# Kernel tuning notes

Measured on AMD Instinct MI355X. Metric: run time of the kernel, lower is better.

Reference implementation:

```python
import jax, jax.numpy as jnp
import numpy as np

DIM = 512
N_HEAD = 4
WIN = (5, 9)

def setup_inputs() -> dict:
    key = jax.random.key(0)
    ks = jax.random.split(key, 9)
    s = DIM ** -0.5
    x = jax.random.normal(ks[0], (1, 8, 60, 108, DIM), jnp.float32)
    Wq = jax.random.normal(ks[1], (DIM, DIM), jnp.float32) * s
    bq = jax.random.normal(ks[2], (DIM,), jnp.float32) * 0.02
    Wk = jax.random.normal(ks[3], (DIM, DIM), jnp.float32) * s
    bk = jax.random.normal(ks[4], (DIM,), jnp.float32) * 0.02
    Wv = jax.random.normal(ks[5], (DIM, DIM), jnp.float32) * s
    bv = jax.random.normal(ks[6], (DIM,), jnp.float32) * 0.02
    Wp = jax.random.normal(ks[7], (DIM, DIM), jnp.float32) * s
    bp = jax.random.normal(ks[8], (DIM,), jnp.float32) * 0.02
    return {"x": x, "Wq": Wq, "bq": bq, "Wk": Wk, "bk": bk,
            "Wv": Wv, "bv": bv, "Wp": Wp, "bp": bp}

def reference(x, Wq, bq, Wk, bk, Wv, bv, Wp, bp):
    b, t, h, w, c = x.shape
    w_h, w_w = WIN
    n_head = N_HEAD
    c_head = c // n_head
    n_wh = -(-h // w_h)
    n_ww = -(-w // w_w)
    new_h, new_w = n_wh * w_h, n_ww * w_w
    pad_b, pad_r = new_h - h, new_w - w
    if pad_b > 0 or pad_r > 0:
        x = jnp.pad(x, ((0, 0), (0, 0), (0, pad_b), (0, pad_r), (0, 0)))
    # torch nn.Linear: y = x @ W.T + b, weight shape (out, in)
    q = jnp.einsum('bthwc,dc->bthwd', x, Wq) + bq
    k = jnp.einsum('bthwc,dc->bthwd', x, Wk) + bk
    v = jnp.einsum('bthwc,dc->bthwd', x, Wv) + bv

    def part(z):
        # (b,t,H,W,c) -> (b, n_windows, n_head, t*w_h*w_w, c_head)
        z = z.reshape(b, t, n_wh, w_h, n_ww, w_w, n_head, c_head)
        z = z.transpose(0, 2, 4, 6, 1, 3, 5, 7)
        return z.reshape(b, n_wh * n_ww, n_head, t * w_h * w_w, c_head)

    qw, kw, vw = part(q), part(k), part(v)
    scale = c_head ** -0.5
    # all (batch, window) attentions batched into one einsum (fused form of the torch double loop)
    scores = jnp.einsum('bwnsc,bwnkc->bwnsk', qw, kw) * scale
    attn = jax.nn.softmax(scores, axis=-1)
    out = jnp.einsum('bwnsk,bwnkc->bwnsc', attn, vw)
    # merge windows back: (b,t,new_h,new_w,c)
    out = out.reshape(b, n_wh, n_ww, n_head, t, w_h, w_w, c_head)
    out = out.transpose(0, 4, 1, 5, 2, 6, 3, 7).reshape(b, t, new_h, new_w, c)
    out = out[:, :, :h, :w, :]
    out = jnp.einsum('bthwc,dc->bthwd', out, Wp) + bp
    return out
```

## Files before the change

### kernel.cpp

```cpp
#include <hip/hip_runtime.h>

typedef _Float16 f16;
typedef _Float16 f16x8 __attribute__((ext_vector_type(8)));
typedef _Float16 f16x4 __attribute__((ext_vector_type(4)));
typedef float f32x4 __attribute__((ext_vector_type(4)));
typedef unsigned int u32;
typedef unsigned int u32x4 __attribute__((ext_vector_type(4)));

#define MFMA16(a, b, c) __builtin_amdgcn_mfma_f32_16x16x32_f16(a, b, c, 0, 0, 0)

__device__ __forceinline__ void async_copy16(f16* lds, const f16* g) {
    __builtin_amdgcn_global_load_lds(
        (const __attribute__((address_space(1))) unsigned int*)g,
        (__attribute__((address_space(3))) unsigned int*)lds,
        16, 0, 0);
}

__global__ __launch_bounds__(256) void prep_convert(
    const float* __restrict__ x, f16* __restrict__ xh,
    const float* __restrict__ Wq, const float* __restrict__ Wk,
    const float* __restrict__ Wv, const float* __restrict__ Wp,
    const float* __restrict__ bq, const float* __restrict__ bk,
    const float* __restrict__ bv,
    f16* __restrict__ Wqkv, f16* __restrict__ Wph, float* __restrict__ bqkv,
    int* __restrict__ tokmap)
{
    if (blockIdx.x < 12960) {
        int i = blockIdx.x * 256 + threadIdx.x;
        f32x4 a = *(const f32x4*)(x + (size_t)i * 8);
        f32x4 b = *(const f32x4*)(x + (size_t)i * 8 + 4);
        f16x8 h = { (f16)a[0], (f16)a[1], (f16)a[2], (f16)a[3],
                    (f16)b[0], (f16)b[1], (f16)b[2], (f16)b[3] };
        *(f16x8*)(xh + (size_t)i * 8) = h;
        return;
    }
    int i = (blockIdx.x - 12960) * 256 + threadIdx.x;
    if (i < 786432) {
        int r = i >> 9, c = i & 511;
        const float* src = (r < 512) ? Wq : (r < 1024) ? Wk : Wv;
        Wqkv[i] = (f16)src[(r & 511) * 512 + c];
    } else if (i < 786432 + 262144) {
        int j = i - 786432;
        Wph[j] = (f16)Wp[j];
    } else if (i < 786432 + 262144 + 1536) {
        int j = i - (786432 + 262144);
        bqkv[j] = (j < 512) ? bq[j] : (j < 1024) ? bk[j - 512] : bv[j - 1024];
    } else if (i < 786432 + 262144 + 1536 + 51840) {
        int j = i - (786432 + 262144 + 1536);
        int t_ = j / 6480, rem = j % 6480;
        int hh = rem / 108, ww = rem % 108;
        int win = (hh / 5) * 12 + (ww / 9);
        int s = t_ * 45 + (hh % 5) * 9 + (ww % 9);
        tokmap[j] = win * 1440 + s;
    }
}

__global__ __launch_bounds__(256, 3) void qkv_gemm(
    const f16* __restrict__ Xh, const f16* __restrict__ W,
    const float* __restrict__ bias, const int* __restrict__ tokmap,
    f16* __restrict__ Qp, f16* __restrict__ Kp, f16* __restrict__ Vp)
{
    __shared__ __align__(16) f16 As[3][128 * 32];
    __shared__ __align__(16) f16 Bs[3][128 * 32];
    const int tid = threadIdx.x;
    const int lane = tid & 63, wid = tid >> 6;
    const int g = lane >> 4, l15 = lane & 15;
    const int wr = wid >> 1, wc = wid & 1;

    const int orig = blockIdx.x;
    const int xcd = orig & 7;
    const int wg = (xcd < 4 ? xcd * 608 : 2432 + (xcd - 4) * 607) + (orig >> 3);
    const int bn = wg % 12;
    const int brow = (wg / 12) * 128;

    const f16* Abase = Xh + (size_t)brow * 512;
    const f16* Bbase = W + (size_t)bn * 128 * 512;

    f32x4 acc[4][4] = {};

    #define QKV_STAGE(buf, step)                                              \
        {                                                                     \
            const int k0_ = (step) * 32;                                      \
            _Pragma("unroll")                                                 \
            for (int rr = 0; rr < 2; ++rr) {                                  \
                int idx = rr * 256 + tid;                                     \
                int row = idx >> 2, ch = idx & 3;                             \
                int sch = ch ^ ((row >> 1) & 3);                              \
                async_copy16(&As[buf][idx * 8],                               \
                             Abase + (size_t)row * 512 + k0_ + sch * 8);      \
                async_copy16(&Bs[buf][idx * 8],                               \
                             Bbase + (size_t)row * 512 + k0_ + sch * 8);      \
            }                                                                 \
        }

    QKV_STAGE(0, 0);
    QKV_STAGE(1, 1);

    int cur = 0;
    for (int t = 0; t < 16; ++t) {
        if (t < 15) asm volatile("s_waitcnt vmcnt(4)" ::: "memory");
        else        asm volatile("s_waitcnt vmcnt(0)" ::: "memory");
        __builtin_amdgcn_s_barrier();
        __builtin_amdgcn_sched_barrier(0);
        if (t + 2 < 16) {
            int stg = cur + 2; if (stg >= 3) stg -= 3;
            QKV_STAGE(stg, t + 2);
        }
        f16x8 a[4], b[4];
        #pragma unroll
        for (int m = 0; m < 4; ++m) {
            int arow = wr * 64 + m * 16 + l15;
            int sl = g ^ ((arow >> 1) & 3);
            a[m] = *(const f16x8*)&As[cur][arow * 32 + sl * 8];
        }
        #pragma unroll
        for (int n = 0; n < 4; ++n) {
            int brw = wc * 64 + n * 16 + l15;
            int sl = g ^ ((brw >> 1) & 3);
            b[n] = *(const f16x8*)&Bs[cur][brw * 32 + sl * 8];
        }
        __builtin_amdgcn_s_setprio(1);
        #pragma unroll
        for (int m = 0; m < 4; ++m)
            #pragma unroll
            for (int n = 0; n < 4; ++n)
                acc[m][n] = MFMA16(a[m], b[n], acc[m][n]);
        __builtin_amdgcn_s_setprio(0);
        __builtin_amdgcn_s_barrier();
        cur = (cur == 2) ? 0 : cur + 1;
    }
    #undef QKV_STAGE

    const int which = bn >> 2, head = bn & 3;
    f16* dst = (which == 0) ? Qp : (which == 1) ? Kp : Vp;
    #pragma unroll
    for (int m = 0; m < 4; ++m) {
        #pragma unroll
        for (int j = 0; j < 4; ++j) {
            int gm = brow + wr * 64 + m * 16 + g * 4 + j;
            size_t obase = ((size_t)(tokmap[gm] + head * 360)) * 128;
            #pragma unroll
            for (int n = 0; n < 4; ++n) {
                int cidx = wc * 64 + n * 16 + l15;
                float v = acc[m][n][j] + bias[bn * 128 + cidx];
                dst[obase + cidx] = (f16)v;
            }
        }
    }
}

__global__ __launch_bounds__(256, 2) void attn_kernel(
    const f16* __restrict__ Qp, const f16* __restrict__ Kp,
    const f16* __restrict__ Vp, f16* __restrict__ AO)
{
    __shared__ __align__(16) f16 Kl[64 * 140];
    __shared__ __align__(16) f16 Vt[128 * 76];
    __shared__ __align__(16) f16 Pl[192 * 76];

    const int tid = threadIdx.x;
    const int lane = tid & 63, wid = tid >> 6;
    const int g = lane >> 4, l15 = lane & 15;
    const int wh = blockIdx.x >> 1;
    const int half = blockIdx.x & 1;
    const int win = wh >> 2, head = wh & 3;
    const int base = wh * 46080;
    const int qbase = half * 192 + wid * 48;

    const float SC2 = 0.08838834764831845f * 1.4426950408889634f;

    f16x8 qf[3][4];
    #pragma unroll
    for (int qi = 0; qi < 3; ++qi)
        #pragma unroll
        for (int c4 = 0; c4 < 4; ++c4)
            qf[qi][c4] = *(const f16x8*)(Qp + base + (qbase + qi * 16 + l15) * 128 + c4 * 32 + g * 8);

    f32x4 o[3][8] = {};
    float l_r[3] = { 0.f, 0.f, 0.f };

    for (int kt = 0; kt < 6; ++kt) {
        #pragma unroll
        for (int it = 0; it < 4; ++it) {
            int idx = it * 256 + tid;
            int krow = idx >> 4, seg = idx & 15;
            f16x8 kv = *(const f16x8*)(Kp + base + (kt * 64 + krow) * 128 + seg * 8);
            *(f16x8*)&Kl[krow * 140 + seg * 8] = kv;
        }
        #pragma unroll
        for (int it = 0; it < 2; ++it) {
            int i2 = it * 256 + tid;
            int kb = i2 >> 6;
            int chp = (i2 & 63) * 2;
            const u32* Vb = (const u32*)(Vp + base);
            u32 d[8];
            #pragma unroll
            for (int i = 0; i < 8; ++i) {
                int kg = kt * 64 + kb * 8 + i;
                d[i] = (kg < 360) ? Vb[kg * 64 + (chp >> 1)] : 0u;
            }
            u32x4 lo, hi;
            #pragma unroll
            for (int jj = 0; jj < 4; ++jj) {
                lo[jj] = (d[2 * jj] & 0xffffu) | (d[2 * jj + 1] << 16);
                hi[jj] = (d[2 * jj] >> 16) | (d[2 * jj + 1] & 0xffff0000u);
            }
            *(u32x4*)&Vt[chp * 76 + kb * 8] = lo;
            *(u32x4*)&Vt[(chp + 1) * 76 + kb * 8] = hi;
        }
        __syncthreads();

        f32x4 sc[4][3] = {};
        __builtin_amdgcn_s_setprio(1);
        #pragma unroll
        for (int c4 = 0; c4 < 4; ++c4) {
            f16x8 ka[4];
            #pragma unroll
            for (int kf = 0; kf < 4; ++kf)
                ka[kf] = *(const f16x8*)&Kl[(kf * 16 + l15) * 140 + c4 * 32 + g * 8];
            #pragma unroll
            for (int kf = 0; kf < 4; ++kf)
                #pragma unroll
                for (int qi = 0; qi < 3; ++qi)
                    sc[kf][qi] = MFMA16(ka[kf], qf[qi][c4], sc[kf][qi]);
        }
        __builtin_amdgcn_s_setprio(0);
        if (kt == 5) {
            #pragma unroll
            for (int kf = 0; kf < 4; ++kf)
                #pragma unroll
                for (int j = 0; j < 4; ++j)
                    if (320 + kf * 16 + g * 4 + j >= 360) {
                        #pragma unroll
                        for (int qi = 0; qi < 3; ++qi) sc[kf][qi][j] = -1e30f;
                    }
        }

        #pragma unroll
        for (int qi = 0; qi < 3; ++qi) {
            float psum = 0.f;
            #pragma unroll
            for (int kf = 0; kf < 4; ++kf) {
                f16x4 pv;
                #pragma unroll
                for (int j = 0; j < 4; ++j) {
                    float p = exp2f(sc[kf][qi][j] * SC2);
                    psum += p;
                    pv[j] = (f16)p;
                }
                *(f16x4*)&Pl[(wid * 48 + qi * 16 + l15) * 76 + kf * 16 + g * 4] = pv;
            }
            psum += __shfl_xor(psum, 16);
            psum += __shfl_xor(psum, 32);
            l_r[qi] += psum;
        }

        __builtin_amdgcn_s_setprio(1);
        #pragma unroll
        for (int kc = 0; kc < 2; ++kc) {
            f16x8 pa[3], vb[8];
            #pragma unroll
            for (int qi = 0; qi < 3; ++qi)
                pa[qi] = *(const f16x8*)&Pl[(wid * 48 + qi * 16 + l15) * 76 + kc * 32 + g * 8];
            #pragma unroll
            for (int chf = 0; chf < 8; ++chf)
                vb[chf] = *(const f16x8*)&Vt[(chf * 16 + l15) * 76 + kc * 32 + g * 8];
            #pragma unroll
            for (int qi = 0; qi < 3; ++qi)
                #pragma unroll
                for (int chf = 0; chf < 8; ++chf)
                    o[qi][chf] = MFMA16(pa[qi], vb[chf], o[qi][chf]);
        }
        __builtin_amdgcn_s_setprio(0);
        __syncthreads();
    }

    #pragma unroll
    for (int qi = 0; qi < 3; ++qi) {
        #pragma unroll
        for (int j = 0; j < 4; ++j) {
            float lj = __shfl(l_r[qi], g * 4 + j);
            float inv = 1.0f / lj;
            int s = qbase + qi * 16 + g * 4 + j;
            if (s < 360) {
                int t_ = s / 45, s45 = s % 45;
                int hh = (win / 12) * 5 + s45 / 9;
                int ww = (win % 12) * 9 + s45 % 9;
                int mm = t_ * 6480 + hh * 108 + ww;
                #pragma unroll
                for (int chf = 0; chf < 8; ++chf) {
                    int col = head * 128 + chf * 16 + l15;
                    AO[(size_t)mm * 512 + col] = (f16)(o[qi][chf][j] * inv);
                }
            }
        }
    }
}

__global__ __launch_bounds__(256, 3) void proj_gemm(
    const f16* __restrict__ A, const f16* __restrict__ W,
    const float* __restrict__ bias, float* __restrict__ out)
{
    __shared__ __align__(16) f16 As[3][128 * 32];
    __shared__ __align__(16) f16 Bs[3][128 * 32];
    const int tid = threadIdx.x;
    const int lane = tid & 63, wid = tid >> 6;
    const int g = lane >> 4, l15 = lane & 15;
    const int wr = wid >> 1, wc = wid & 1;

    const int orig = blockIdx.x;
    const int xcd = orig & 7;
    const int wg = (xcd < 4 ? xcd * 203 : 812 + (xcd - 4) * 202) + (orig >> 3);
    const int bcol = (wg & 3) * 128;
    const int brow = (wg >> 2) * 128;

    const f16* Abase = A + (size_t)brow * 512;
    const f16* Bbase = W + (size_t)bcol * 512;

    f32x4 acc[4][4] = {};

    #define PROJ_STAGE(buf, step)                                             \
        {                                                                     \
            const int k0_ = (step) * 32;                                      \
            _Pragma("unroll")                                                 \
            for (int rr = 0; rr < 2; ++rr) {                                  \
                int idx = rr * 256 + tid;                                     \
                int row = idx >> 2, ch = idx & 3;                             \
                int sch = ch ^ ((row >> 1) & 3);                              \
                async_copy16(&As[buf][idx * 8],                               \
                             Abase + (size_t)row * 512 + k0_ + sch * 8);      \
                async_copy16(&Bs[buf][idx * 8],                               \
                             Bbase + (size_t)row * 512 + k0_ + sch * 8);      \
            }                                                                 \
        }

    PROJ_STAGE(0, 0);
    PROJ_STAGE(1, 1);

    int cur = 0;
    for (int t = 0; t < 16; ++t) {
        if (t < 15) asm volatile("s_waitcnt vmcnt(4)" ::: "memory");
        else        asm volatile("s_waitcnt vmcnt(0)" ::: "memory");
        __builtin_amdgcn_s_barrier();
        __builtin_amdgcn_sched_barrier(0);
        if (t + 2 < 16) {
            int stg = cur + 2; if (stg >= 3) stg -= 3;
            PROJ_STAGE(stg, t + 2);
        }
        f16x8 a[4], b[4];
        #pragma unroll
        for (int m = 0; m < 4; ++m) {
            int arow = wr * 64 + m * 16 + l15;
            int sl = g ^ ((arow >> 1) & 3);
            a[m] = *(const f16x8*)&As[cur][arow * 32 + sl * 8];
        }
        #pragma unroll
        for (int n = 0; n < 4; ++n) {
            int brw = wc * 64 + n * 16 + l15;
            int sl = g ^ ((brw >> 1) & 3);
            b[n] = *(const f16x8*)&Bs[cur][brw * 32 + sl * 8];
        }
        __builtin_amdgcn_s_setprio(1);
        #pragma unroll
        for (int m = 0; m < 4; ++m)
            #pragma unroll
            for (int n = 0; n < 4; ++n)
                acc[m][n] = MFMA16(a[m], b[n], acc[m][n]);
        __builtin_amdgcn_s_setprio(0);
        __builtin_amdgcn_s_barrier();
        cur = (cur == 2) ? 0 : cur + 1;
    }
    #undef PROJ_STAGE

    #pragma unroll
    for (int m = 0; m < 4; ++m)
        #pragma unroll
        for (int j = 0; j < 4; ++j) {
            int gm = brow + wr * 64 + m * 16 + g * 4 + j;
            #pragma unroll
            for (int n = 0; n < 4; ++n) {
                int gn = bcol + wc * 64 + n * 16 + l15;
                out[(size_t)gm * 512 + gn] = acc[m][n][j] + bias[gn];
            }
        }
}

extern "C" void kernel_launch(void* const* d_in, const int* in_sizes, int n_in,
                              void* d_out, int out_size, void* d_ws, size_t ws_size,
                              hipStream_t stream)
{
    (void)in_sizes; (void)n_in; (void)out_size; (void)ws_size;
    const float* x  = (const float*)d_in[0];
    const float* Wq = (const float*)d_in[1];
    const float* bq = (const float*)d_in[2];
    const float* Wk = (const float*)d_in[3];
    const float* bk = (const float*)d_in[4];
    const float* Wv = (const float*)d_in[5];
    const float* bv = (const float*)d_in[6];
    const float* Wp = (const float*)d_in[7];
    const float* bp = (const float*)d_in[8];

    f16* Qp   = (f16*)d_ws;
    f16* Kp   = Qp + 26542080;
    f16* Vp   = Kp + 26542080;
    f16* AO   = Vp + 26542080;
    f16* xh   = AO;
    f16* Wqkv = AO + 26542080;
    f16* Wph  = Wqkv + 786432;
    float* bqkv = (float*)(Wph + 262144);
    int* tokmap = (int*)(bqkv + 1536);

    prep_convert<<<17265, 256, 0, stream>>>(x, xh, Wq, Wk, Wv, Wp, bq, bk, bv,
                                            Wqkv, Wph, bqkv, tokmap);
    qkv_gemm<<<4860, 256, 0, stream>>>(xh, Wqkv, bqkv, tokmap, Qp, Kp, Vp);
    attn_kernel<<<1152, 256, 0, stream>>>(Qp, Kp, Vp, AO);
    proj_gemm<<<1620, 256, 0, stream>>>(AO, Wph, bp, (float*)d_out);
}
```

Measured before the change: 267.7 us.

## Fuse fp32-to-fp16 input conversion into QKV GEMM tile loads

Removes the separate pass that converted x to fp16 and instead streams fp32 x tiles directly into LDS inside the QKV GEMM, converting to fp16 when building MFMA fragments. This eliminates a full read/write pass over the activation tensor and one kernel's worth of work. In exchange the GEMM reads twice as many bytes for A per tile, uses more LDS with a new swizzle, and its occupancy hint drops from 3 to 2 blocks per CU.

```diff
diff --git a/kernel.cpp b/kernel.cpp
--- a/kernel.cpp
+++ b/kernel.cpp
@@ -9,15 +9,14 @@
 
 #define MFMA16(a, b, c) __builtin_amdgcn_mfma_f32_16x16x32_f16(a, b, c, 0, 0, 0)
 
-__device__ __forceinline__ void async_copy16(f16* lds, const f16* g) {
+__device__ __forceinline__ void async_copy16(const void* g, void* lds) {
     __builtin_amdgcn_global_load_lds(
         (const __attribute__((address_space(1))) unsigned int*)g,
         (__attribute__((address_space(3))) unsigned int*)lds,
         16, 0, 0);
 }
 
-__global__ __launch_bounds__(256) void prep_convert(
-    const float* __restrict__ x, f16* __restrict__ xh,
+__global__ __launch_bounds__(256) void prep_kernel(
     const float* __restrict__ Wq, const float* __restrict__ Wk,
     const float* __restrict__ Wv, const float* __restrict__ Wp,
     const float* __restrict__ bq, const float* __restrict__ bk,
@@ -25,16 +24,7 @@
     f16* __restrict__ Wqkv, f16* __restrict__ Wph, float* __restrict__ bqkv,
     int* __restrict__ tokmap)
 {
-    if (blockIdx.x < 12960) {
-        int i = blockIdx.x * 256 + threadIdx.x;
-        f32x4 a = *(const f32x4*)(x + (size_t)i * 8);
-        f32x4 b = *(const f32x4*)(x + (size_t)i * 8 + 4);
-        f16x8 h = { (f16)a[0], (f16)a[1], (f16)a[2], (f16)a[3],
-                    (f16)b[0], (f16)b[1], (f16)b[2], (f16)b[3] };
-        *(f16x8*)(xh + (size_t)i * 8) = h;
-        return;
-    }
-    int i = (blockIdx.x - 12960) * 256 + threadIdx.x;
+    int i = blockIdx.x * 256 + threadIdx.x;
     if (i < 786432) {
         int r = i >> 9, c = i & 511;
         const float* src = (r < 512) ? Wq : (r < 1024) ? Wk : Wv;
@@ -55,12 +45,12 @@
     }
 }
 
-__global__ __launch_bounds__(256, 3) void qkv_gemm(
-    const f16* __restrict__ Xh, const f16* __restrict__ W,
+__global__ __launch_bounds__(256, 2) void qkv_gemm(
+    const float* __restrict__ X, const f16* __restrict__ W,
     const float* __restrict__ bias, const int* __restrict__ tokmap,
     f16* __restrict__ Qp, f16* __restrict__ Kp, f16* __restrict__ Vp)
 {
-    __shared__ __align__(16) f16 As[3][128 * 32];
+    __shared__ __align__(16) float Af[3][128 * 32];
     __shared__ __align__(16) f16 Bs[3][128 * 32];
     const int tid = threadIdx.x;
     const int lane = tid & 63, wid = tid >> 6;
@@ -73,7 +63,7 @@
     const int bn = wg % 12;
     const int brow = (wg / 12) * 128;
 
-    const f16* Abase = Xh + (size_t)brow * 512;
+    const float* Abase = X + (size_t)brow * 512;
     const f16* Bbase = W + (size_t)bn * 128 * 512;
 
     f32x4 acc[4][4] = {};
@@ -81,15 +71,21 @@
     #define QKV_STAGE(buf, step)                                              \
         {                                                                     \
             const int k0_ = (step) * 32;                                      \
+            _Pragma("unroll")                                                 \
+            for (int rr = 0; rr < 4; ++rr) {                                  \
+                int idx = rr * 256 + tid;                                     \
+                int row = idx >> 3, sl = idx & 7;                             \
+                int ss = sl ^ (row & 7);                                      \
+                async_copy16(Abase + (size_t)row * 512 + k0_ + ss * 4,        \
+                             &Af[buf][idx * 4]);                              \
+            }                                                                 \
             _Pragma("unroll")                                                 \
             for (int rr = 0; rr < 2; ++rr) {                                  \
                 int idx = rr * 256 + tid;                                     \
                 int row = idx >> 2, ch = idx & 3;                             \
                 int sch = ch ^ ((row >> 1) & 3);                              \
-                async_copy16(&As[buf][idx * 8],                               \
-                             Abase + (size_t)row * 512 + k0_ + sch * 8);      \
-                async_copy16(&Bs[buf][idx * 8],                               \
-                             Bbase + (size_t)row * 512 + k0_ + sch * 8);      \
+                async_copy16(Bbase + (size_t)row * 512 + k0_ + sch * 8,       \
+                             &Bs[buf][idx * 8]);                              \
             }                                                                 \
         }
 
@@ -98,7 +94,7 @@
 
     int cur = 0;
     for (int t = 0; t < 16; ++t) {
-        if (t < 15) asm volatile("s_waitcnt vmcnt(4)" ::: "memory");
+        if (t < 15) asm volatile("s_waitcnt vmcnt(6)" ::: "memory");
         else        asm volatile("s_waitcnt vmcnt(0)" ::: "memory");
         __builtin_amdgcn_s_barrier();
         __builtin_amdgcn_sched_barrier(0);
@@ -110,8 +106,12 @@
         #pragma unroll
         for (int m = 0; m < 4; ++m) {
             int arow = wr * 64 + m * 16 + l15;
-            int sl = g ^ ((arow >> 1) & 3);
-            a[m] = *(const f16x8*)&As[cur][arow * 32 + sl * 8];
+            int s0 = (2 * g) ^ (arow & 7);
+            int s1 = (2 * g + 1) ^ (arow & 7);
+            f32x4 lo = *(const f32x4*)&Af[cur][arow * 32 + s0 * 4];
+            f32x4 hi = *(const f32x4*)&Af[cur][arow * 32 + s1 * 4];
+            a[m] = f16x8{ (f16)lo[0], (f16)lo[1], (f16)lo[2], (f16)lo[3],
+                          (f16)hi[0], (f16)hi[1], (f16)hi[2], (f16)hi[3] };
         }
         #pragma unroll
         for (int n = 0; n < 4; ++n) {
@@ -326,10 +326,10 @@
                 int idx = rr * 256 + tid;                                     \
                 int row = idx >> 2, ch = idx & 3;                             \
                 int sch = ch ^ ((row >> 1) & 3);                              \
-                async_copy16(&As[buf][idx * 8],                               \
-                             Abase + (size_t)row * 512 + k0_ + sch * 8);      \
-                async_copy16(&Bs[buf][idx * 8],                               \
-                             Bbase + (size_t)row * 512 + k0_ + sch * 8);      \
+                async_copy16(Abase + (size_t)row * 512 + k0_ + sch * 8,       \
+                             &As[buf][idx * 8]);                              \
+                async_copy16(Bbase + (size_t)row * 512 + k0_ + sch * 8,       \
+                             &Bs[buf][idx * 8]);                              \
             }                                                                 \
         }
 
@@ -403,15 +403,14 @@
     f16* Kp   = Qp + 26542080;
     f16* Vp   = Kp + 26542080;
     f16* AO   = Vp + 26542080;
-    f16* xh   = AO;
     f16* Wqkv = AO + 26542080;
     f16* Wph  = Wqkv + 786432;
     float* bqkv = (float*)(Wph + 262144);
     int* tokmap = (int*)(bqkv + 1536);
 
-    prep_convert<<<17265, 256, 0, stream>>>(x, xh, Wq, Wk, Wv, Wp, bq, bk, bv,
-                                            Wqkv, Wph, bqkv, tokmap);
-    qkv_gemm<<<4860, 256, 0, stream>>>(xh, Wqkv, bqkv, tokmap, Qp, Kp, Vp);
+    prep_kernel<<<4305, 256, 0, stream>>>(Wq, Wk, Wv, Wp, bq, bk, bv,
+                                          Wqkv, Wph, bqkv, tokmap);
+    qkv_gemm<<<4860, 256, 0, stream>>>(x, Wqkv, bqkv, tokmap, Qp, Kp, Vp);
     attn_kernel<<<1152, 256, 0, stream>>>(Qp, Kp, Vp, AO);
     proj_gemm<<<1620, 256, 0, stream>>>(AO, Wph, bp, (float*)d_out);
 }
```

After: 358.6 us. +33.9%, slower.
